# Kernel tuning notes

Hardware: AMD Instinct MI355X
Metric: run time of the kernel (lower is better)

## Reference

```python
import jax, jax.numpy as jnp
import numpy as np

N, E, G = 50000, 500000, 64
DIN, D, OUT, L = 64, 128, 10, 3


def setup_inputs() -> dict:
    key = jax.random.key(0)
    ks = iter(jax.random.split(key, 32))

    def nrm(shape, scale=0.05):
        return jax.random.normal(next(ks), shape, dtype=jnp.float32) * scale

    x = jax.random.normal(next(ks), (N, DIN), dtype=jnp.float32)
    edge_index = jax.random.randint(next(ks), (2, E), 0, N)
    batch = jnp.sort(jax.random.randint(next(ks), (N,), 0, G))
    return {
        "x": x,
        "edge_index": edge_index,
        "batch": batch,
        "num_graphs": G,
        # GIN encoder (gnn_node): input proj + L GIN layers (MLP: D->2D->D)
        "enc_in_W": nrm((DIN, D)), "enc_in_b": nrm((D,)),
        "enc_W1": nrm((L, D, 2 * D)), "enc_b1": nrm((L, 2 * D)),
        "enc_W2": nrm((L, 2 * D, D)), "enc_b2": nrm((L, D)),
        # edge attention MLP: Linear(2D, 4D) -> ReLU -> Linear(4D, 1)
        "att_W1": nrm((2 * D, 4 * D)), "att_b1": nrm((4 * D,)),
        "att_W2": nrm((4 * D, 1)), "att_b2": nrm((1,)),
        # classifier GNN on raw x (c_in='raw'), edge-weight-masked GIN
        "clf_in_W": nrm((DIN, D)), "clf_in_b": nrm((D,)),
        "clf_W1": nrm((L, D, 2 * D)), "clf_b1": nrm((L, 2 * D)),
        "clf_W2": nrm((L, 2 * D, D)), "clf_b2": nrm((L, D)),
        # prediction head after mean pooling
        "head_W": nrm((D, OUT)), "head_b": nrm((OUT,)),
    }


def reference(x, edge_index, batch, num_graphs,
              enc_in_W, enc_in_b, enc_W1, enc_b1, enc_W2, enc_b2,
              att_W1, att_b1, att_W2, att_b2,
              clf_in_W, clf_in_b, clf_W1, clf_b1, clf_W2, clf_b2,
              head_W, head_b):
    row, col = edge_index[0], edge_index[1]
    n = x.shape[0]

    def gin_layer(h, W1, b1, W2, b2, ew=None):
        msg = h[col]                         # gather [E, D]
        if ew is not None:
            msg = msg * ew[:, None]          # masked message passing
        agg = jax.ops.segment_sum(msg, row, num_segments=n)  # scatter-add [N, D]
        z = agg + h                          # (1 + eps) * h with eps = 0
        return jax.nn.relu(z @ W1 + b1) @ W2 + b2

    # ---- gnn_encoder: unweighted GIN over full graph ----
    h = jax.nn.relu(x @ enc_in_W + enc_in_b)
    nl = enc_W1.shape[0]
    for l in range(nl):
        h = gin_layer(h, enc_W1[l], enc_b1[l], enc_W2[l], enc_b2[l])
        if l < nl - 1:
            h = jax.nn.relu(h)

    # ---- edge attention MLP on [h_row, h_col] ----
    edge_rep = jnp.concatenate([h[row], h[col]], axis=-1)  # [E, 2D]
    logit = (jax.nn.relu(edge_rep @ att_W1 + att_b1) @ att_W2 + att_b2).reshape(-1)
    att = jax.nn.sigmoid(logit)  # concrete_sample, eval mode (deterministic)

    # ---- classifier GNN on raw x with edge-weight masks (set_masks) ----
    hc = jax.nn.relu(x @ clf_in_W + clf_in_b)
    for l in range(nl):
        hc = gin_layer(hc, clf_W1[l], clf_b1[l], clf_W2[l], clf_b2[l], ew=att)
        if l < nl - 1:
            hc = jax.nn.relu(hc)

    # ---- mean pooling per graph + linear head ----
    sums = jax.ops.segment_sum(hc, batch, num_segments=num_graphs)
    cnt = jax.ops.segment_sum(jnp.ones((n, 1), hc.dtype), batch, num_segments=num_graphs)
    pooled = sums / jnp.maximum(cnt, 1.0)
    return pooled @ head_W + head_b  # causal_pred [G, OUT]
```

## Files before the change

kernel.cpp:

```cpp
#include <hip/hip_runtime.h>
#include <hip/hip_bf16.h>
#include <cstddef>

#define kN 50000
#define kNP 50048
#define kE 500000
#define kG 64
#define kDIN 64
#define kD 128
#define kH 256
#define kA4 512
#define kOUT 10
#define PCHUNK 200
#define SBLK 196

typedef __attribute__((ext_vector_type(8))) short bfrag_t;
typedef __attribute__((ext_vector_type(4))) float f32x4;
typedef __attribute__((ext_vector_type(2))) float f32x2;
union FragCast { uint4 u; bfrag_t f; };

__device__ __attribute__((aligned(16))) __hip_bfloat16 g_h [(size_t)kNP * kD];
__device__ __attribute__((aligned(16))) __hip_bfloat16 g_hc[(size_t)kNP * kD];
__device__ __attribute__((aligned(16))) __hip_bfloat16 g_z [(size_t)kNP * kD];
__device__ __attribute__((aligned(16))) __hip_bfloat16 g_A [(size_t)kNP * kA4];
__device__ __attribute__((aligned(16))) unsigned char  g_Bf8[(size_t)kNP * kA4];
__device__ __attribute__((aligned(16))) __hip_bfloat16 g_pk[1056 * 512];
__device__ float g_atts[kE];
__device__ int   g_rowptr[kN + 1];
__device__ int   g_cnt[kN];
__device__ int   g_tmp[SBLK * 256];
__device__ int   g_bsum[256];
__device__ int   g_cols[kE];
__device__ float g_pool[kG * kD];
__device__ float g_gcnt[kG];

__device__ inline float bflo(unsigned u) { union { unsigned i; float f; } c; c.i = u << 16; return c.f; }
__device__ inline float bfhi(unsigned u) { union { unsigned i; float f; } c; c.i = u & 0xffff0000u; return c.f; }
__device__ inline __hip_bfloat16* bsel(int s) { return s == 0 ? g_h : (s == 1 ? g_hc : g_z); }

struct SrcPtrs { const float* p[16]; };

__global__ __launch_bounds__(64) void prepack_kernel(SrcPtrs sp) {
    const int fs[17] = {0,64,128,192,256,320,384,448,512,576,640,704,768,896,1024,1040,1056};
    const int Ns[16] = {256,256,256,128,128,128,256,256,256,128,128,128,512,512,128,128};
    int f = blockIdx.x;
    int m = 0;
    while (f >= fs[m + 1]) m++;
    const int fl = f - fs[m];
    const int N = Ns[m];
    const int n0 = fl % (N >> 4);
    const int k0 = fl / (N >> 4);
    const int lane = threadIdx.x;
    const int q = lane >> 4, c = lane & 15;
    const float* src = sp.p[m];
    __hip_bfloat16* dst = g_pk + (size_t)f * 512 + lane * 8;
    const int kb = k0 * 32 + q * 8;
    const int n = n0 * 16 + c;
#pragma unroll
    for (int j = 0; j < 8; j++)
        dst[j] = __float2bfloat16(src[(size_t)(kb + j) * N + n]);
}

#define PK_ENC_W1(l) ((size_t)(0   + (l) * 64) * 512)
#define PK_ENC_W2(l) ((size_t)(192 + (l) * 64) * 512)
#define PK_CLF_W1(l) ((size_t)(384 + (l) * 64) * 512)
#define PK_CLF_W2(l) ((size_t)(576 + (l) * 64) * 512)
#define PK_ATT_TOP   ((size_t)768 * 512)
#define PK_ATT_BOT   ((size_t)896 * 512)
#define PK_ENC_IN    ((size_t)1024 * 512)
#define PK_CLF_IN    ((size_t)1040 * 512)

__global__ __launch_bounds__(256) void zero_prep_kernel() {
    const int i = blockIdx.x * 256 + threadIdx.x;
    if (i < kN) g_cnt[i] = 0;
    if (i < kG * kD) g_pool[i] = 0.f;
    if (i < kG) g_gcnt[i] = 0.f;
}

__global__ __launch_bounds__(256) void hist_kernel(const int* __restrict__ row) {
    const int e = blockIdx.x * 256 + threadIdx.x;
    if (e < kE) atomicAdd(&g_cnt[row[e]], 1);
}

__global__ __launch_bounds__(256) void scan1_kernel() {
    __shared__ int sh[256];
    const int t = threadIdx.x;
    const int i = blockIdx.x * 256 + t;
    const int c = (i < kN) ? g_cnt[i] : 0;
    sh[t] = c;
    __syncthreads();
    int v = c;
    for (int off = 1; off < 256; off <<= 1) {
        int add = (t >= off) ? sh[t - off] : 0;
        __syncthreads();
        v += add;
        sh[t] = v;
        __syncthreads();
    }
    g_tmp[i] = v - c;
    if (t == 255) g_bsum[blockIdx.x] = v;
}

__global__ __launch_bounds__(256) void scan2_kernel() {
    __shared__ int sh[256];
    const int t = threadIdx.x;
    const int c = (t < SBLK) ? g_bsum[t] : 0;
    sh[t] = c;
    __syncthreads();
    int v = c;
    for (int off = 1; off < 256; off <<= 1) {
        int add = (t >= off) ? sh[t - off] : 0;
        __syncthreads();
        v += add;
        sh[t] = v;
        __syncthreads();
    }
    if (t < SBLK) g_bsum[t] = v - c;
}

__global__ __launch_bounds__(256) void scan3_kernel() {
    const int i = blockIdx.x * 256 + threadIdx.x;
    const int v = g_tmp[i] + g_bsum[blockIdx.x];
    if (i <= kN) g_rowptr[i] = v;
    if (i < kN) g_cnt[i] = v;
}

__global__ __launch_bounds__(256) void scatter_kernel(
    const int* __restrict__ row, const int* __restrict__ col) {
    const int e = blockIdx.x * 256 + threadIdx.x;
    if (e >= kE) return;
    const int r = row[e];
    const int pos = atomicAdd(&g_cnt[r], 1);
    g_cols[pos] = col[e];
}

__global__ __launch_bounds__(256) void input_proj_mfma(
    const float* __restrict__ x,
    const float* __restrict__ eb, const float* __restrict__ cb) {
    __shared__ __hip_bfloat16 xs[64][72];
    __shared__ __hip_bfloat16 ob[64][264];
    const int t = threadIdx.x, lane = t & 63, w = t >> 6;
    const int node0 = blockIdx.x * 64;
#pragma unroll
    for (int it = 0; it < 4; it++) {
        int idx = t + it * 256;
        int r = idx >> 4, c = idx & 15;
        float4 v = make_float4(0.f, 0.f, 0.f, 0.f);
        if (node0 + r < kN) v = ((const float4*)x)[(size_t)(node0 + r) * 16 + c];
        union { uint2 u; __hip_bfloat16 h[4]; } o;
        o.h[0] = __float2bfloat16(v.x); o.h[1] = __float2bfloat16(v.y);
        o.h[2] = __float2bfloat16(v.z); o.h[3] = __float2bfloat16(v.w);
        *(uint2*)(&xs[r][c * 4]) = o.u;
    }
    __syncthreads();
    const int q = lane >> 4, cidx = lane & 15;
    f32x4 acc[4][4] = {};
    const uint4* pk = (const uint4*)(g_pk + (w >= 2 ? PK_CLF_IN : PK_ENC_IN));
#pragma unroll
    for (int k0 = 0; k0 < 2; k0++) {
        FragCast a[4], b[4];
#pragma unroll
        for (int mt = 0; mt < 4; mt++)
            a[mt].u = *(const uint4*)(&xs[mt * 16 + cidx][k0 * 32 + q * 8]);
#pragma unroll
        for (int nt = 0; nt < 4; nt++)
            b[nt].u = pk[(size_t)(k0 * 8 + (w & 1) * 4 + nt) * 64 + lane];
#pragma unroll
        for (int mt = 0; mt < 4; mt++)
#pragma unroll
            for (int nt = 0; nt < 4; nt++)
                acc[mt][nt] = __builtin_amdgcn_mfma_f32_16x16x32_bf16(
                    a[mt].f, b[nt].f, acc[mt][nt], 0, 0, 0);
    }
    const float* bp = (w >= 2) ? cb : eb;
#pragma unroll
    for (int nt = 0; nt < 4; nt++) {
        const int mcol = (w & 1) * 64 + nt * 16 + cidx;
        const float bv = bp[mcol];
#pragma unroll
        for (int mt = 0; mt < 4; mt++)
#pragma unroll
            for (int r = 0; r < 4; r++)
                ob[mt * 16 + q * 4 + r][w * 64 + nt * 16 + cidx] =
                    __float2bfloat16(fmaxf(acc[mt][nt][r] + bv, 0.f));
    }
    __syncthreads();
#pragma unroll
    for (int it = 0; it < 8; it++) {
        int idx = t + it * 256;
        int r = idx >> 5, c = idx & 31;
        uint4 v = *(const uint4*)(&ob[r][c * 8]);
        if (c < 16) ((uint4*)(g_h  + (size_t)(node0 + r) * kD))[c]      = v;
        else        ((uint4*)(g_hc + (size_t)(node0 + r) * kD))[c - 16] = v;
    }
}

#define AGG_ACC(v, wt) \
    a0 = fmaf(bflo(v.x), wt, a0); a1 = fmaf(bfhi(v.x), wt, a1); \
    a2 = fmaf(bflo(v.y), wt, a2); a3 = fmaf(bfhi(v.y), wt, a3); \
    a4 = fmaf(bflo(v.z), wt, a4); a5 = fmaf(bfhi(v.z), wt, a5); \
    a6 = fmaf(bflo(v.w), wt, a6); a7 = fmaf(bfhi(v.w), wt, a7);
#define AGG_SUM(v) \
    a0 += bflo(v.x); a1 += bfhi(v.x); a2 += bflo(v.y); a3 += bfhi(v.y); \
    a4 += bflo(v.z); a5 += bfhi(v.z); a6 += bflo(v.w); a7 += bfhi(v.w);

__global__ __launch_bounds__(256) void agg_csr_kernel(int src_sel, int use_att) {
    const int t = threadIdx.x;
    const int node = blockIdx.x * 16 + (t >> 4);
    const int li = t & 15;
    const uint4* __restrict__ src = (const uint4*)bsel(src_sel);
    float a0 = 0.f, a1 = 0.f, a2 = 0.f, a3 = 0.f, a4 = 0.f, a5 = 0.f, a6 = 0.f, a7 = 0.f;
    if (node < kN) {
        const uint4 sv = src[(size_t)node * 16 + li];
        a0 = bflo(sv.x); a1 = bfhi(sv.x); a2 = bflo(sv.y); a3 = bfhi(sv.y);
        a4 = bflo(sv.z); a5 = bfhi(sv.z); a6 = bflo(sv.w); a7 = bfhi(sv.w);
        const int beg = g_rowptr[node], end = g_rowptr[node + 1];
        int j = beg;
        if (use_att) {
            for (; j + 4 <= end; j += 4) {
                uint4 v0 = src[(size_t)g_cols[j    ] * 16 + li];
                uint4 v1 = src[(size_t)g_cols[j + 1] * 16 + li];
                uint4 v2 = src[(size_t)g_cols[j + 2] * 16 + li];
                uint4 v3 = src[(size_t)g_cols[j + 3] * 16 + li];
                const float w0 = g_atts[j],     w1 = g_atts[j + 1];
                const float w2 = g_atts[j + 2], w3 = g_atts[j + 3];
                AGG_ACC(v0, w0) AGG_ACC(v1, w1) AGG_ACC(v2, w2) AGG_ACC(v3, w3)
            }
            for (; j < end; j++) {
                const uint4 v = src[(size_t)g_cols[j] * 16 + li];
                const float wt = g_atts[j];
                AGG_ACC(v, wt)
            }
        } else {
            for (; j + 4 <= end; j += 4) {
                uint4 v0 = src[(size_t)g_cols[j    ] * 16 + li];
                uint4 v1 = src[(size_t)g_cols[j + 1] * 16 + li];
                uint4 v2 = src[(size_t)g_cols[j + 2] * 16 + li];
                uint4 v3 = src[(size_t)g_cols[j + 3] * 16 + li];
                AGG_SUM(v0) AGG_SUM(v1) AGG_SUM(v2) AGG_SUM(v3)
            }
            for (; j < end; j++) {
                const uint4 v = src[(size_t)g_cols[j] * 16 + li];
                AGG_SUM(v)
            }
        }
    }
    union { uint4 u; __hip_bfloat16 h[8]; } o;
    o.h[0] = __float2bfloat16(a0); o.h[1] = __float2bfloat16(a1);
    o.h[2] = __float2bfloat16(a2); o.h[3] = __float2bfloat16(a3);
    o.h[4] = __float2bfloat16(a4); o.h[5] = __float2bfloat16(a5);
    o.h[6] = __float2bfloat16(a6); o.h[7] = __float2bfloat16(a7);
    ((uint4*)g_z)[(size_t)node * 16 + li] = o.u;
}

__global__ __launch_bounds__(256) void gin_mlp_mfma(
    int dst_sel, size_t pkW1off, size_t pkW2off,
    const float* __restrict__ b1, const float* __restrict__ b2, int relu_out) {
    __shared__ __hip_bfloat16 zs[64][136];
    __shared__ __hip_bfloat16 hid[64][264];
    const int t = threadIdx.x, lane = t & 63, w = t >> 6;
    const int node0 = blockIdx.x * 64;
    __hip_bfloat16* hp = bsel(dst_sel);

    {
        const uint4* src = (const uint4*)(g_z + (size_t)node0 * kD);
#pragma unroll
        for (int it = 0; it < 4; it++) {
            int idx = t + it * 256;
            int r = idx >> 4, c = idx & 15;
            *(uint4*)(&zs[r][c * 8]) = src[(size_t)r * 16 + c];
        }
    }
    __syncthreads();

    const int q = lane >> 4, cidx = lane & 15;

    f32x4 acc1[4][4] = {};
    const uint4* pk1 = (const uint4*)(g_pk + pkW1off);
    for (int k0 = 0; k0 < 4; k0++) {
        FragCast a[4], b[4];
#pragma unroll
        for (int mt = 0; mt < 4; mt++)
            a[mt].u = *(const uint4*)(&zs[mt * 16 + cidx][k0 * 32 + q * 8]);
#pragma unroll
        for (int nt = 0; nt < 4; nt++)
            b[nt].u = pk1[(size_t)(k0 * 16 + (w * 4 + nt)) * 64 + lane];
#pragma unroll
        for (int mt = 0; mt < 4; mt++)
#pragma unroll
            for (int nt = 0; nt < 4; nt++)
                acc1[mt][nt] = __builtin_amdgcn_mfma_f32_16x16x32_bf16(
                    a[mt].f, b[nt].f, acc1[mt][nt], 0, 0, 0);
    }
#pragma unroll
    for (int nt = 0; nt < 4; nt++) {
        const int col = w * 64 + nt * 16 + cidx;
        const float bv = b1[col];
#pragma unroll
        for (int mt = 0; mt < 4; mt++)
#pragma unroll
            for (int r = 0; r < 4; r++)
                hid[mt * 16 + q * 4 + r][col] =
                    __float2bfloat16(fmaxf(acc1[mt][nt][r] + bv, 0.f));
    }
    __syncthreads();

    f32x4 acc2[4][2] = {};
    const uint4* pk2 = (const uint4*)(g_pk + pkW2off);
    for (int k0 = 0; k0 < 8; k0++) {
        FragCast a[4], b[2];
#pragma unroll
        for (int mt = 0; mt < 4; mt++)
            a[mt].u = *(const uint4*)(&hid[mt * 16 + cidx][k0 * 32 + q * 8]);
#pragma unroll
        for (int nt = 0; nt < 2; nt++)
            b[nt].u = pk2[(size_t)(k0 * 8 + (w * 2 + nt)) * 64 + lane];
#pragma unroll
        for (int mt = 0; mt < 4; mt++)
#pragma unroll
            for (int nt = 0; nt < 2; nt++)
                acc2[mt][nt] = __builtin_amdgcn_mfma_f32_16x16x32_bf16(
                    a[mt].f, b[nt].f, acc2[mt][nt], 0, 0, 0);
    }
#pragma unroll
    for (int nt = 0; nt < 2; nt++) {
        const int col = w * 32 + nt * 16 + cidx;
        const float bv = b2[col];
#pragma unroll
        for (int mt = 0; mt < 4; mt++)
#pragma unroll
            for (int r = 0; r < 4; r++) {
                float v = acc2[mt][nt][r] + bv;
                if (relu_out) v = fmaxf(v, 0.f);
                zs[mt * 16 + q * 4 + r][col] = __float2bfloat16(v);
            }
    }
    __syncthreads();
    {
        uint4* dst = (uint4*)(hp + (size_t)node0 * kD);
#pragma unroll
        for (int it = 0; it < 4; it++) {
            int idx = t + it * 256;
            int r = idx >> 4, c = idx & 15;
            dst[(size_t)r * 16 + c] = *(const uint4*)(&zs[r][c * 8]);
        }
    }
}

__global__ __launch_bounds__(256) void att_dense_mfma(const float* __restrict__ b1) {
    __shared__ __hip_bfloat16 zs[64][136];
    __shared__ __hip_bfloat16 ob[64][264];
    const int t = threadIdx.x, lane = t & 63, w = t >> 6;
    const int node0 = blockIdx.x * 64;
    const int mat = blockIdx.y >> 1, half = blockIdx.y & 1;
    const size_t pkoff = mat ? PK_ATT_BOT : PK_ATT_TOP;

    const uint4* src = (const uint4*)(g_h + (size_t)node0 * kD);
#pragma unroll
    for (int it = 0; it < 4; it++) {
        int idx = t + it * 256;
        int r = idx >> 4, c = idx & 15;
        *(uint4*)(&zs[r][c * 8]) = src[(size_t)r * 16 + c];
    }
    __syncthreads();

    const int q = lane >> 4, cidx = lane & 15;
    f32x4 acc[4][4] = {};
    const uint4* pk = (const uint4*)(g_pk + pkoff);
    for (int k0 = 0; k0 < 4; k0++) {
        FragCast a[4], b[4];
#pragma unroll
        for (int mt = 0; mt < 4; mt++)
            a[mt].u = *(const uint4*)(&zs[mt * 16 + cidx][k0 * 32 + q * 8]);
#pragma unroll
        for (int nt = 0; nt < 4; nt++)
            b[nt].u = pk[(size_t)(k0 * 32 + (half * 16 + w * 4 + nt)) * 64 + lane];
#pragma unroll
        for (int mt = 0; mt < 4; mt++)
#pragma unroll
            for (int nt = 0; nt < 4; nt++)
                acc[mt][nt] = __builtin_amdgcn_mfma_f32_16x16x32_bf16(
                    a[mt].f, b[nt].f, acc[mt][nt], 0, 0, 0);
    }
#pragma unroll
    for (int nt = 0; nt < 4; nt++) {
        const int lcol = w * 64 + nt * 16 + cidx;
        const float bv = (mat == 0) ? b1[half * 256 + lcol] : 0.f;
#pragma unroll
        for (int mt = 0; mt < 4; mt++)
#pragma unroll
            for (int r = 0; r < 4; r++)
                ob[mt * 16 + q * 4 + r][lcol] = __float2bfloat16(acc[mt][nt][r] + bv);
    }
    __syncthreads();
    if (mat == 0) {
        uint4* dst = (uint4*)(g_A + (size_t)node0 * kA4 + half * 256);
#pragma unroll
        for (int it = 0; it < 8; it++) {
            int idx = t + it * 256;
            int r = idx >> 5, c = idx & 31;
            dst[(size_t)r * 64 + c] = *(const uint4*)(&ob[r][c * 8]);
        }
    } else {
        uint2* dst = (uint2*)(g_Bf8 + (size_t)node0 * kA4 + half * 256);
#pragma unroll
        for (int it = 0; it < 8; it++) {
            int idx = t + it * 256;
            int r = idx >> 5, c = idx & 31;
            union { uint4 u; __hip_bfloat16 h[8]; } iv;
            iv.u = *(const uint4*)(&ob[r][c * 8]);
            float f[8];
#pragma unroll
            for (int i = 0; i < 8; i++) f[i] = __bfloat162float(iv.h[i]);
            int w0 = __builtin_amdgcn_cvt_pk_fp8_f32(f[0], f[1], 0, false);
            w0 = __builtin_amdgcn_cvt_pk_fp8_f32(f[2], f[3], w0, true);
            int w1 = __builtin_amdgcn_cvt_pk_fp8_f32(f[4], f[5], 0, false);
            w1 = __builtin_amdgcn_cvt_pk_fp8_f32(f[6], f[7], w1, true);
            uint2 o;
            o.x = (unsigned)w0;
            o.y = (unsigned)w1;
            dst[(size_t)r * 64 + c] = o;
        }
    }
}

__device__ inline float edge_dot16_f8(const f32x2* a2, const f32x2* w2, uint4 bu) {
    const f32x2 zero = {0.f, 0.f};
    f32x2 p = zero;
    const unsigned wd[4] = {bu.x, bu.y, bu.z, bu.w};
#pragma unroll
    for (int k = 0; k < 4; k++) {
        f32x2 b0 = __builtin_amdgcn_cvt_pk_f32_fp8(wd[k], false);
        f32x2 b1 = __builtin_amdgcn_cvt_pk_f32_fp8(wd[k], true);
        f32x2 t0 = __builtin_elementwise_max(a2[2 * k] + b0, zero);
        f32x2 t1 = __builtin_elementwise_max(a2[2 * k + 1] + b1, zero);
        p = p + t0 * w2[2 * k];
        p = p + t1 * w2[2 * k + 1];
    }
    return p.x + p.y;
}

__global__ __launch_bounds__(256) void att_edge_csr(
    const float* __restrict__ W2, const float* __restrict__ b2) {
    const int node = blockIdx.x * 4 + (threadIdx.x >> 6);
    const int lane = threadIdx.x & 63;
    const int sub = lane >> 5;
    const int li  = lane & 31;
    const int m0 = li * 16;
    const uint4 au0 = *(const uint4*)(g_A + (size_t)node * kA4 + m0);
    const uint4 au1 = *(const uint4*)(g_A + (size_t)node * kA4 + m0 + 8);
    f32x2 a2[8];
    a2[0] = (f32x2){bflo(au0.x), bfhi(au0.x)};
    a2[1] = (f32x2){bflo(au0.y), bfhi(au0.y)};
    a2[2] = (f32x2){bflo(au0.z), bfhi(au0.z)};
    a2[3] = (f32x2){bflo(au0.w), bfhi(au0.w)};
    a2[4] = (f32x2){bflo(au1.x), bfhi(au1.x)};
    a2[5] = (f32x2){bflo(au1.y), bfhi(au1.y)};
    a2[6] = (f32x2){bflo(au1.z), bfhi(au1.z)};
    a2[7] = (f32x2){bflo(au1.w), bfhi(au1.w)};
    f32x2 w2[8];
#pragma unroll
    for (int k = 0; k < 8; k++) {
        const float2 wk = *(const float2*)(W2 + m0 + 2 * k);
        w2[k] = (f32x2){wk.x, wk.y};
    }
    const float bb = b2[0];
    const int beg = g_rowptr[node], end = g_rowptr[node + 1];

    int j = beg;
    for (; j + 4 <= end; j += 4) {
        const int c0 = g_cols[j + sub];
        const int c1 = g_cols[j + 2 + sub];
        const uint4 b0 = *(const uint4*)(g_Bf8 + (size_t)c0 * kA4 + m0);
        const uint4 b1 = *(const uint4*)(g_Bf8 + (size_t)c1 * kA4 + m0);
        float s0 = edge_dot16_f8(a2, w2, b0);
        float s1 = edge_dot16_f8(a2, w2, b1);
        for (int off = 16; off > 0; off >>= 1) {
            s0 += __shfl_down(s0, off);
            s1 += __shfl_down(s1, off);
        }
        if (li == 0) {
            g_atts[j + sub]     = 1.f / (1.f + __expf(-(s0 + bb)));
            g_atts[j + 2 + sub] = 1.f / (1.f + __expf(-(s1 + bb)));
        }
    }
    for (; j < end; j += 2) {
        const int je = j + sub;
        const int jc = (je < end) ? je : (end - 1);
        const int c = g_cols[jc];
        const uint4 b0 = *(const uint4*)(g_Bf8 + (size_t)c * kA4 + m0);
        float s = edge_dot16_f8(a2, w2, b0);
        for (int off = 16; off > 0; off >>= 1) s += __shfl_down(s, off);
        if (li == 0 && je < end)
            g_atts[je] = 1.f / (1.f + __expf(-(s + bb)));
    }
}

__global__ __launch_bounds__(64) void pool_kernel(const int* __restrict__ batch) {
    const int t = threadIdx.x;
    int n = blockIdx.x * PCHUNK;
    const int nend = n + PCHUNK;
    const unsigned* __restrict__ hc = (const unsigned*)g_hc;
    int gcur = batch[n];
    float a0 = 0.f, a1 = 0.f, cv = 0.f;
    for (; n < nend; n++) {
        const int g = batch[n];
        if (g != gcur) {
            atomicAdd(&g_pool[gcur * kD + 2 * t], a0);
            atomicAdd(&g_pool[gcur * kD + 2 * t + 1], a1);
            if (t == 0) atomicAdd(&g_gcnt[gcur], cv);
            a0 = a1 = cv = 0.f; gcur = g;
        }
        unsigned v = hc[(size_t)n * 64 + t];
        a0 += bflo(v); a1 += bfhi(v);
        cv += 1.f;
    }
    atomicAdd(&g_pool[gcur * kD + 2 * t], a0);
    atomicAdd(&g_pool[gcur * kD + 2 * t + 1], a1);
    if (t == 0) atomicAdd(&g_gcnt[gcur], cv);
}

__global__ __launch_bounds__(640) void head_kernel(
    const float* __restrict__ hW, const float* __restrict__ hb,
    float* __restrict__ out) {
    const int t = threadIdx.x;
    const int g = t / kOUT, o = t - g * kOUT;
    const float c = fmaxf(g_gcnt[g], 1.f);
    const float inv = 1.f / c;
    float acc = hb[o];
    for (int k = 0; k < kD; k++)
        acc = fmaf(g_pool[g * kD + k] * inv, hW[k * kOUT + o], acc);
    out[(size_t)g * kOUT + o] = acc;
}

extern "C" void kernel_launch(void* const* d_in, const int* in_sizes, int n_in,
                              void* d_out, int out_size, void* d_ws, size_t ws_size,
                              hipStream_t stream) {
    const float* x        = (const float*)d_in[0];
    const int*   ei       = (const int*)d_in[1];
    const int*   row      = ei;
    const int*   col      = ei + kE;
    const int*   batch    = (const int*)d_in[2];
    const float* enc_in_W = (const float*)d_in[4];
    const float* enc_in_b = (const float*)d_in[5];
    const float* enc_W1   = (const float*)d_in[6];
    const float* enc_b1   = (const float*)d_in[7];
    const float* enc_W2   = (const float*)d_in[8];
    const float* enc_b2   = (const float*)d_in[9];
    const float* att_W1   = (const float*)d_in[10];
    const float* att_b1   = (const float*)d_in[11];
    const float* att_W2   = (const float*)d_in[12];
    const float* att_b2   = (const float*)d_in[13];
    const float* clf_in_W = (const float*)d_in[14];
    const float* clf_in_b = (const float*)d_in[15];
    const float* clf_W1   = (const float*)d_in[16];
    const float* clf_b1   = (const float*)d_in[17];
    const float* clf_W2   = (const float*)d_in[18];
    const float* clf_b2   = (const float*)d_in[19];
    const float* head_W   = (const float*)d_in[20];
    const float* head_b   = (const float*)d_in[21];
    float* out = (float*)d_out;

    const dim3 blk(256);
    const int eblocks = (kE + 255) / 256;

    SrcPtrs sp;
    for (int l = 0; l < 3; l++) {
        sp.p[0 + l] = enc_W1 + (size_t)l * kD * kH;
        sp.p[3 + l] = enc_W2 + (size_t)l * kH * kD;
        sp.p[6 + l] = clf_W1 + (size_t)l * kD * kH;
        sp.p[9 + l] = clf_W2 + (size_t)l * kH * kD;
    }
    sp.p[12] = att_W1;
    sp.p[13] = att_W1 + (size_t)kD * kA4;
    sp.p[14] = enc_in_W;
    sp.p[15] = clf_in_W;
    prepack_kernel<<<1056, dim3(64), 0, stream>>>(sp);

    zero_prep_kernel<<<(kN + 255) / 256, blk, 0, stream>>>();
    hist_kernel<<<eblocks, blk, 0, stream>>>(row);
    scan1_kernel<<<SBLK, blk, 0, stream>>>();
    scan2_kernel<<<1, blk, 0, stream>>>();
    scan3_kernel<<<SBLK, blk, 0, stream>>>();
    scatter_kernel<<<eblocks, blk, 0, stream>>>(row, col);

    input_proj_mfma<<<kNP / 64, blk, 0, stream>>>(x, enc_in_b, clf_in_b);

    for (int l = 0; l < 3; l++) {
        agg_csr_kernel<<<kNP / 16, blk, 0, stream>>>(0, 0);
        gin_mlp_mfma<<<kNP / 64, blk, 0, stream>>>(
            0, PK_ENC_W1(l), PK_ENC_W2(l),
            enc_b1 + (size_t)l * kH, enc_b2 + (size_t)l * kD, (l < 2) ? 1 : 0);
    }

    att_dense_mfma<<<dim3(kNP / 64, 4), blk, 0, stream>>>(att_b1);
    att_edge_csr<<<kN / 4, blk, 0, stream>>>(att_W2, att_b2);

    for (int l = 0; l < 3; l++) {
        agg_csr_kernel<<<kNP / 16, blk, 0, stream>>>(1, 1);
        gin_mlp_mfma<<<kNP / 64, blk, 0, stream>>>(
            1, PK_CLF_W1(l), PK_CLF_W2(l),
            clf_b1 + (size_t)l * kH, clf_b2 + (size_t)l * kD, (l < 2) ? 1 : 0);
    }

    pool_kernel<<<kN / PCHUNK, dim3(64), 0, stream>>>(batch);
    head_kernel<<<1, dim3(kG * kOUT), 0, stream>>>(head_W, head_b, out);
}
```

Measured before the change: 614.8 us.

## Gather neighbor features in fp8 shadow copies during GIN aggregation

Every producer of node features (input projection and GIN MLP epilogues) now also writes an fp8 copy of the features. The CSR aggregation kernel gathers neighbor rows from these fp8 copies, which halves the bytes per random gather, and accumulates with packed float2 ops. The edge-attention kernel also gets an 8-edge unrolled loop for more memory-level parallelism. The trade is extra writes of the fp8 arrays and reduced precision in the aggregated messages.

```diff
diff --git a/kernel.cpp b/kernel.cpp
--- a/kernel.cpp
+++ b/kernel.cpp
@@ -22,6 +22,8 @@
 __device__ __attribute__((aligned(16))) __hip_bfloat16 g_h [(size_t)kNP * kD];
 __device__ __attribute__((aligned(16))) __hip_bfloat16 g_hc[(size_t)kNP * kD];
 __device__ __attribute__((aligned(16))) __hip_bfloat16 g_z [(size_t)kNP * kD];
+__device__ __attribute__((aligned(16))) unsigned char  g_h8 [(size_t)kNP * kD];
+__device__ __attribute__((aligned(16))) unsigned char  g_hc8[(size_t)kNP * kD];
 __device__ __attribute__((aligned(16))) __hip_bfloat16 g_A [(size_t)kNP * kA4];
 __device__ __attribute__((aligned(16))) unsigned char  g_Bf8[(size_t)kNP * kA4];
 __device__ __attribute__((aligned(16))) __hip_bfloat16 g_pk[1056 * 512];
@@ -37,6 +39,18 @@
 __device__ inline float bflo(unsigned u) { union { unsigned i; float f; } c; c.i = u << 16; return c.f; }
 __device__ inline float bfhi(unsigned u) { union { unsigned i; float f; } c; c.i = u & 0xffff0000u; return c.f; }
 __device__ inline __hip_bfloat16* bsel(int s) { return s == 0 ? g_h : (s == 1 ? g_hc : g_z); }
+
+__device__ inline uint2 bf8pack(uint4 v) {
+    float f[8];
+    f[0] = bflo(v.x); f[1] = bfhi(v.x); f[2] = bflo(v.y); f[3] = bfhi(v.y);
+    f[4] = bflo(v.z); f[5] = bfhi(v.z); f[6] = bflo(v.w); f[7] = bfhi(v.w);
+    int w0 = __builtin_amdgcn_cvt_pk_fp8_f32(f[0], f[1], 0, false);
+    w0 = __builtin_amdgcn_cvt_pk_fp8_f32(f[2], f[3], w0, true);
+    int w1 = __builtin_amdgcn_cvt_pk_fp8_f32(f[4], f[5], 0, false);
+    w1 = __builtin_amdgcn_cvt_pk_fp8_f32(f[6], f[7], w1, true);
+    uint2 o; o.x = (unsigned)w0; o.y = (unsigned)w1;
+    return o;
+}
 
 struct SrcPtrs { const float* p[16]; };
 
@@ -190,66 +204,85 @@
         int idx = t + it * 256;
         int r = idx >> 5, c = idx & 31;
         uint4 v = *(const uint4*)(&ob[r][c * 8]);
-        if (c < 16) ((uint4*)(g_h  + (size_t)(node0 + r) * kD))[c]      = v;
-        else        ((uint4*)(g_hc + (size_t)(node0 + r) * kD))[c - 16] = v;
-    }
-}
-
-#define AGG_ACC(v, wt) \
-    a0 = fmaf(bflo(v.x), wt, a0); a1 = fmaf(bfhi(v.x), wt, a1); \
-    a2 = fmaf(bflo(v.y), wt, a2); a3 = fmaf(bfhi(v.y), wt, a3); \
-    a4 = fmaf(bflo(v.z), wt, a4); a5 = fmaf(bfhi(v.z), wt, a5); \
-    a6 = fmaf(bflo(v.w), wt, a6); a7 = fmaf(bfhi(v.w), wt, a7);
-#define AGG_SUM(v) \
-    a0 += bflo(v.x); a1 += bfhi(v.x); a2 += bflo(v.y); a3 += bfhi(v.y); \
-    a4 += bflo(v.z); a5 += bfhi(v.z); a6 += bflo(v.w); a7 += bfhi(v.w);
+        uint2 v8 = bf8pack(v);
+        if (c < 16) {
+            ((uint4*)(g_h  + (size_t)(node0 + r) * kD))[c] = v;
+            ((uint2*)(g_h8 + (size_t)(node0 + r) * kD))[c] = v8;
+        } else {
+            ((uint4*)(g_hc  + (size_t)(node0 + r) * kD))[c - 16] = v;
+            ((uint2*)(g_hc8 + (size_t)(node0 + r) * kD))[c - 16] = v8;
+        }
+    }
+}
+
+__device__ inline void f8acc(uint2 v, f32x2 wt, f32x2& c0, f32x2& c1, f32x2& c2, f32x2& c3) {
+    c0 = c0 + __builtin_amdgcn_cvt_pk_f32_fp8(v.x, false) * wt;
+    c1 = c1 + __builtin_amdgcn_cvt_pk_f32_fp8(v.x, true)  * wt;
+    c2 = c2 + __builtin_amdgcn_cvt_pk_f32_fp8(v.y, false) * wt;
+    c3 = c3 + __builtin_amdgcn_cvt_pk_f32_fp8(v.y, true)  * wt;
+}
+__device__ inline void f8sum(uint2 v, f32x2& c0, f32x2& c1, f32x2& c2, f32x2& c3) {
+    c0 = c0 + __builtin_amdgcn_cvt_pk_f32_fp8(v.x, false);
+    c1 = c1 + __builtin_amdgcn_cvt_pk_f32_fp8(v.x, true);
+    c2 = c2 + __builtin_amdgcn_cvt_pk_f32_fp8(v.y, false);
+    c3 = c3 + __builtin_amdgcn_cvt_pk_f32_fp8(v.y, true);
+}
 
 __global__ __launch_bounds__(256) void agg_csr_kernel(int src_sel, int use_att) {
     const int t = threadIdx.x;
     const int node = blockIdx.x * 16 + (t >> 4);
     const int li = t & 15;
-    const uint4* __restrict__ src = (const uint4*)bsel(src_sel);
-    float a0 = 0.f, a1 = 0.f, a2 = 0.f, a3 = 0.f, a4 = 0.f, a5 = 0.f, a6 = 0.f, a7 = 0.f;
+    const uint4* __restrict__ src  = (const uint4*)bsel(src_sel);
+    const uint2* __restrict__ src8 = (const uint2*)(src_sel == 0 ? g_h8 : g_hc8);
+    f32x2 c0 = {0.f, 0.f}, c1 = {0.f, 0.f}, c2 = {0.f, 0.f}, c3 = {0.f, 0.f};
     if (node < kN) {
         const uint4 sv = src[(size_t)node * 16 + li];
-        a0 = bflo(sv.x); a1 = bfhi(sv.x); a2 = bflo(sv.y); a3 = bfhi(sv.y);
-        a4 = bflo(sv.z); a5 = bfhi(sv.z); a6 = bflo(sv.w); a7 = bfhi(sv.w);
+        c0 = (f32x2){bflo(sv.x), bfhi(sv.x)};
+        c1 = (f32x2){bflo(sv.y), bfhi(sv.y)};
+        c2 = (f32x2){bflo(sv.z), bfhi(sv.z)};
+        c3 = (f32x2){bflo(sv.w), bfhi(sv.w)};
         const int beg = g_rowptr[node], end = g_rowptr[node + 1];
         int j = beg;
         if (use_att) {
             for (; j + 4 <= end; j += 4) {
-                uint4 v0 = src[(size_t)g_cols[j    ] * 16 + li];
-                uint4 v1 = src[(size_t)g_cols[j + 1] * 16 + li];
-                uint4 v2 = src[(size_t)g_cols[j + 2] * 16 + li];
-                uint4 v3 = src[(size_t)g_cols[j + 3] * 16 + li];
+                const uint2 v0 = src8[(size_t)g_cols[j    ] * 16 + li];
+                const uint2 v1 = src8[(size_t)g_cols[j + 1] * 16 + li];
+                const uint2 v2 = src8[(size_t)g_cols[j + 2] * 16 + li];
+                const uint2 v3 = src8[(size_t)g_cols[j + 3] * 16 + li];
                 const float w0 = g_atts[j],     w1 = g_atts[j + 1];
                 const float w2 = g_atts[j + 2], w3 = g_atts[j + 3];
-                AGG_ACC(v0, w0) AGG_ACC(v1, w1) AGG_ACC(v2, w2) AGG_ACC(v3, w3)
+                f8acc(v0, (f32x2){w0, w0}, c0, c1, c2, c3);
+                f8acc(v1, (f32x2){w1, w1}, c0, c1, c2, c3);
+                f8acc(v2, (f32x2){w2, w2}, c0, c1, c2, c3);
+                f8acc(v3, (f32x2){w3, w3}, c0, c1, c2, c3);
             }
             for (; j < end; j++) {
-                const uint4 v = src[(size_t)g_cols[j] * 16 + li];
+                const uint2 v = src8[(size_t)g_cols[j] * 16 + li];
                 const float wt = g_atts[j];
-                AGG_ACC(v, wt)
+                f8acc(v, (f32x2){wt, wt}, c0, c1, c2, c3);
             }
         } else {
             for (; j + 4 <= end; j += 4) {
-                uint4 v0 = src[(size_t)g_cols[j    ] * 16 + li];
-                uint4 v1 = src[(size_t)g_cols[j + 1] * 16 + li];
-                uint4 v2 = src[(size_t)g_cols[j + 2] * 16 + li];
-                uint4 v3 = src[(size_t)g_cols[j + 3] * 16 + li];
-                AGG_SUM(v0) AGG_SUM(v1) AGG_SUM(v2) AGG_SUM(v3)
+                const uint2 v0 = src8[(size_t)g_cols[j    ] * 16 + li];
+                const uint2 v1 = src8[(size_t)g_cols[j + 1] * 16 + li];
+                const uint2 v2 = src8[(size_t)g_cols[j + 2] * 16 + li];
+                const uint2 v3 = src8[(size_t)g_cols[j + 3] * 16 + li];
+                f8sum(v0, c0, c1, c2, c3);
+                f8sum(v1, c0, c1, c2, c3);
+                f8sum(v2, c0, c1, c2, c3);
+                f8sum(v3, c0, c1, c2, c3);
             }
             for (; j < end; j++) {
-                const uint4 v = src[(size_t)g_cols[j] * 16 + li];
-                AGG_SUM(v)
+                const uint2 v = src8[(size_t)g_cols[j] * 16 + li];
+                f8sum(v, c0, c1, c2, c3);
             }
         }
     }
     union { uint4 u; __hip_bfloat16 h[8]; } o;
-    o.h[0] = __float2bfloat16(a0); o.h[1] = __float2bfloat16(a1);
-    o.h[2] = __float2bfloat16(a2); o.h[3] = __float2bfloat16(a3);
-    o.h[4] = __float2bfloat16(a4); o.h[5] = __float2bfloat16(a5);
-    o.h[6] = __float2bfloat16(a6); o.h[7] = __float2bfloat16(a7);
+    o.h[0] = __float2bfloat16(c0.x); o.h[1] = __float2bfloat16(c0.y);
+    o.h[2] = __float2bfloat16(c1.x); o.h[3] = __float2bfloat16(c1.y);
+    o.h[4] = __float2bfloat16(c2.x); o.h[5] = __float2bfloat16(c2.y);
+    o.h[6] = __float2bfloat16(c3.x); o.h[7] = __float2bfloat16(c3.y);
     ((uint4*)g_z)[(size_t)node * 16 + li] = o.u;
 }
 
@@ -261,6 +294,7 @@
     const int t = threadIdx.x, lane = t & 63, w = t >> 6;
     const int node0 = blockIdx.x * 64;
     __hip_bfloat16* hp = bsel(dst_sel);
+    unsigned char* mp = dst_sel == 0 ? g_h8 : g_hc8;
 
     {
         const uint4* src = (const uint4*)(g_z + (size_t)node0 * kD);
@@ -338,11 +372,14 @@
     __syncthreads();
     {
         uint4* dst = (uint4*)(hp + (size_t)node0 * kD);
+        uint2* md  = (uint2*)(mp + (size_t)node0 * kD);
 #pragma unroll
         for (int it = 0; it < 4; it++) {
             int idx = t + it * 256;
             int r = idx >> 4, c = idx & 15;
-            dst[(size_t)r * 16 + c] = *(const uint4*)(&zs[r][c * 8]);
+            uint4 v = *(const uint4*)(&zs[r][c * 8]);
+            dst[(size_t)r * 16 + c] = v;
+            md[(size_t)r * 16 + c] = bf8pack(v);
         }
     }
 }
@@ -407,19 +444,7 @@
         for (int it = 0; it < 8; it++) {
             int idx = t + it * 256;
             int r = idx >> 5, c = idx & 31;
-            union { uint4 u; __hip_bfloat16 h[8]; } iv;
-            iv.u = *(const uint4*)(&ob[r][c * 8]);
-            float f[8];
-#pragma unroll
-            for (int i = 0; i < 8; i++) f[i] = __bfloat162float(iv.h[i]);
-            int w0 = __builtin_amdgcn_cvt_pk_fp8_f32(f[0], f[1], 0, false);
-            w0 = __builtin_amdgcn_cvt_pk_fp8_f32(f[2], f[3], w0, true);
-            int w1 = __builtin_amdgcn_cvt_pk_fp8_f32(f[4], f[5], 0, false);
-            w1 = __builtin_amdgcn_cvt_pk_fp8_f32(f[6], f[7], w1, true);
-            uint2 o;
-            o.x = (unsigned)w0;
-            o.y = (unsigned)w1;
-            dst[(size_t)r * 64 + c] = o;
+            dst[(size_t)r * 64 + c] = bf8pack(*(const uint4*)(&ob[r][c * 8]));
         }
     }
 }
@@ -468,6 +493,32 @@
     const int beg = g_rowptr[node], end = g_rowptr[node + 1];
 
     int j = beg;
+    for (; j + 8 <= end; j += 8) {
+        const int c0 = g_cols[j + sub];
+        const int c1 = g_cols[j + 2 + sub];
+        const int c2 = g_cols[j + 4 + sub];
+        const int c3 = g_cols[j + 6 + sub];
+        const uint4 b0 = *(const uint4*)(g_Bf8 + (size_t)c0 * kA4 + m0);
+        const uint4 b1 = *(const uint4*)(g_Bf8 + (size_t)c1 * kA4 + m0);
+        const uint4 b2v = *(const uint4*)(g_Bf8 + (size_t)c2 * kA4 + m0);
+        const uint4 b3 = *(const uint4*)(g_Bf8 + (size_t)c3 * kA4 + m0);
+        float s0 = edge_dot16_f8(a2, w2, b0);
+        float s1 = edge_dot16_f8(a2, w2, b1);
+        float s2 = edge_dot16_f8(a2, w2, b2v);
+        float s3 = edge_dot16_f8(a2, w2, b3);
+        for (int off = 16; off > 0; off >>= 1) {
+            s0 += __shfl_down(s0, off);
+            s1 += __shfl_down(s1, off);
+            s2 += __shfl_down(s2, off);
+            s3 += __shfl_down(s3, off);
+        }
+        if (li == 0) {
+            g_atts[j + sub]     = 1.f / (1.f + __expf(-(s0 + bb)));
+            g_atts[j + 2 + sub] = 1.f / (1.f + __expf(-(s1 + bb)));
+            g_atts[j + 4 + sub] = 1.f / (1.f + __expf(-(s2 + bb)));
+            g_atts[j + 6 + sub] = 1.f / (1.f + __expf(-(s3 + bb)));
+        }
+    }
     for (; j + 4 <= end; j += 4) {
         const int c0 = g_cols[j + sub];
         const int c1 = g_cols[j + 2 + sub];
```

Result: faster. 574.4 us (-6.6%).
